# Kernel tuning notes

Hardware: AMD Instinct MI355X
Metric: run time of the kernel (lower is better)

Reference implementation:

```python
import jax, jax.numpy as jnp
import numpy as np

# Grid / physics constants (stand-ins for the attributes of self.model)
N = 256                 # voxels per axis (cubic unit cell)
CELL = 100.0            # unit cell edge in Angstrom (orthogonal cell, frac matrix = I/CELL)
SPACING = CELL / N      # voxel spacing in Angstrom
SOLVENT_R = 1.1         # dilation probe radius (init default `radius`)
EROSION_R = 0.9         # erosion radius (init default `erosion_radius`)
VDW_MAX = 1.9           # static upper bound on vdw radii (generation range [1.2,1.9])
N_ATOMS = 5000


def setup_inputs() -> dict:
    key = jax.random.key(0)
    k1, k2 = jax.random.split(key)
    xyz = jax.random.uniform(k1, (N_ATOMS, 3), jnp.float32) * CELL
    vdw_radii = 1.2 + 0.7 * jax.random.uniform(k2, (N_ATOMS,), jnp.float32)
    return {"xyz": xyz, "vdw_radii": vdw_radii}


def _solvent_pipeline(xyz, vdw_radii):
    # ---- Step 1: dilation -- per-atom radius query into the voxel grid ----
    max_r = VDW_MAX + SOLVENT_R                       # self.max_radius_angstrom
    Kh = int(np.ceil(max_r / SPACING))
    g = np.arange(-Kh, Kh + 1)
    offs = np.stack(np.meshgrid(g, g, g, indexing='ij'), -1).reshape(-1, 3)
    offs = jnp.asarray(offs, jnp.int32)               # [M,3] local voxel offsets

    base = jnp.floor(xyz / SPACING).astype(jnp.int32)          # [A,3] home voxel
    coords = base[:, None, :] + offs[None, :, :]               # [A,M,3]
    centers = coords.astype(jnp.float32) * SPACING             # voxel centers (unwrapped)
    d = jnp.sqrt(jnp.sum((centers - xyz[:, None, :]) ** 2, -1))  # [A,M] atom-voxel dist

    w = jnp.mod(coords, N)                                     # periodic wrap of indices
    flat = ((w[..., 0] * N + w[..., 1]) * N + w[..., 2]).ravel()

    vr = vdw_radii[:, None]
    prot = (d < vr).ravel()                                    # inside vdw -> protein core
    bound = ((d >= vr) & (d < vr + SOLVENT_R)).ravel()         # vdw..vdw+probe -> boundary

    protein = (jnp.zeros(N ** 3, jnp.int8).at[flat].max(prot.astype(jnp.int8)) > 0)
    boundary = (jnp.zeros(N ** 3, jnp.int8).at[flat].max(bound.astype(jnp.int8)) > 0)
    protein = protein.reshape(N, N, N)
    boundary = boundary.reshape(N, N, N) & ~protein            # symmetry = identity (P1)
    def_solv = ~(protein | boundary)

    # ---- Step 2: erosion -- boundary voxel flips to solvent if any voxel within
    #      erosion_radius is definitely solvent ----
    rh = int(np.ceil(EROSION_R / SPACING))
    g2 = np.arange(-rh, rh + 1)
    eo = np.stack(np.meshgrid(g2, g2, g2, indexing='ij'), -1).reshape(-1, 3)
    eo = eo[np.linalg.norm(eo * SPACING, axis=1) <= EROSION_R]  # sphere stencil (static)
    has_nb = jnp.zeros((N, N, N), bool)
    for o in eo:  # small static stencil (~50 offsets)
        has_nb = has_nb | jnp.roll(def_solv, shift=(-int(o[0]), -int(o[1]), -int(o[2])), axis=(0, 1, 2))
    flip = boundary & has_nb
    protein_with_boundary = (protein | boundary) & ~flip
    solvent = (~protein_with_boundary).astype(jnp.float32)

    # ---- Step 3: Gaussian smoothing with circular padding ----
    sigma = (SOLVENT_R / SPACING) / 4.0                        # self.transition (voxels)
    ks = int(4 * sigma + 1)
    if ks % 2 == 0:
        ks += 1
    x = np.arange(ks) - ks // 2
    g1 = np.exp(-x ** 2 / (2 * sigma ** 2))
    g1 = g1 / g1.sum()
    k3 = g1[:, None, None] * g1[None, :, None] * g1[None, None, :]
    k3 = jnp.asarray(k3 / k3.sum(), jnp.float32)
    pad = ks // 2
    padded = jnp.pad(solvent, pad, mode='wrap')
    out = jax.lax.conv_general_dilated(padded[None, None], k3[None, None], (1, 1, 1), 'VALID')
    return out[0, 0]  # [N,N,N] smoothed solvent mask


def reference(xyz, vdw_radii):
    return _solvent_pipeline(xyz, vdw_radii)
```

## Files before the change

kernel.cpp:

```cpp
#include <hip/hip_runtime.h>
#include <math.h>

#define NG 256
#define NG3 (NG*NG*NG)
#define NW (NG3/64)

typedef unsigned long long u64;
typedef unsigned int u32;

constexpr float SPACING_F = 0.390625f;
constexpr int KH = 8;
constexpr int KD = 17;
constexpr int NPAIR = KD * KD;

#define CB(x, y) (((((x) & 255) << 8) | ((y) & 255)) << 2)

__global__ void __launch_bounds__(256) splat_bits_kernel(
    const float* __restrict__ xyz, const float* __restrict__ vdw,
    u64* __restrict__ occ_bits, u64* __restrict__ p_bits, int natoms)
{
    int t = blockIdx.x * 256 + threadIdx.x;
    if (t >= natoms * NPAIR) return;
    int atom = t / NPAIR;
    int pr = t - atom * NPAIR;
    int dx = pr / KD - KH;
    int dy = pr - (pr / KD) * KD - KH;

    const float ax = xyz[atom * 3 + 0];
    const float ay = xyz[atom * 3 + 1];
    const float az = xyz[atom * 3 + 2];
    const float vr = vdw[atom];
    const float br = __fadd_rn(vr, 1.1f);
    const int bx = (int)floorf(__fdiv_rn(ax, SPACING_F));
    const int by = (int)floorf(__fdiv_rn(ay, SPACING_F));
    const int bz = (int)floorf(__fdiv_rn(az, SPACING_F));

    const int cx = bx + dx, cy = by + dy;
    float ex = __fsub_rn(__fmul_rn((float)cx, SPACING_F), ax);
    float ey = __fsub_rn(__fmul_rn((float)cy, SPACING_F), ay);
    float rxy2 = __fadd_rn(__fmul_rn(ex, ex), __fmul_rn(ey, ey));
    if (rxy2 >= __fmul_rn(br, br)) return;

    u32 mo = 0, mp = 0;
    #pragma unroll
    for (int k = 0; k < KD; ++k) {
        int cz = bz + k - KH;
        float ez = __fsub_rn(__fmul_rn((float)cz, SPACING_F), az);
        float s = __fadd_rn(rxy2, __fmul_rn(ez, ez));
        float d = __fsqrt_rn(s);
        mo |= (d < br) ? (1u << k) : 0u;
        mp |= (d < vr) ? (1u << k) : 0u;
    }
    if (!mo) return;

    const int cb = CB(cx, cy);
    const int zA = (bz - KH) & 255;
    const int wa = zA >> 6;
    const int off = zA & 63;

    u64 lo = (u64)mo << off;
    u64 hi = off ? ((u64)mo >> (64 - off)) : 0ULL;
    if (lo) atomicOr(&occ_bits[cb | wa], lo);
    if (hi) atomicOr(&occ_bits[cb | ((wa + 1) & 3)], hi);
    if (mp) {
        u64 plo = (u64)mp << off;
        u64 phi = off ? ((u64)mp >> (64 - off)) : 0ULL;
        if (plo) atomicOr(&p_bits[cb | wa], plo);
        if (phi) atomicOr(&p_bits[cb | ((wa + 1) & 3)], phi);
    }
}

__device__ __forceinline__ u64 rng5(const u64* __restrict__ B, int cb, int wz) {
    u64 C = B[cb | wz], P = B[cb | ((wz + 3) & 3)], Nw = B[cb | ((wz + 1) & 3)];
    u64 d1 = (C << 1) | (P >> 63), d2 = (C << 2) | (P >> 62);
    u64 u1 = (C >> 1) | (Nw << 63), u2 = (C >> 2) | (Nw << 62);
    return C & d1 & d2 & u1 & u2;
}
__device__ __forceinline__ u64 rng3(const u64* __restrict__ B, int cb, int wz) {
    u64 C = B[cb | wz], P = B[cb | ((wz + 3) & 3)], Nw = B[cb | ((wz + 1) & 3)];
    u64 d1 = (C << 1) | (P >> 63);
    u64 u1 = (C >> 1) | (Nw << 63);
    return C & d1 & u1;
}

__global__ void __launch_bounds__(256) solvent_bits_kernel(
    const u64* __restrict__ occ_bits, const u64* __restrict__ p_bits,
    u64* __restrict__ sol_bits)
{
    int w = blockIdx.x * 256 + threadIdx.x;
    int wz = w & 3, col = w >> 2;
    int y = col & 255, x = col >> 8;

    u64 ero = rng5(occ_bits, CB(x, y), wz);
    ero &= rng5(occ_bits, CB(x + 1, y), wz);
    ero &= rng5(occ_bits, CB(x - 1, y), wz);
    ero &= rng5(occ_bits, CB(x, y + 1), wz);
    ero &= rng5(occ_bits, CB(x, y - 1), wz);
    ero &= rng3(occ_bits, CB(x + 1, y + 1), wz);
    ero &= rng3(occ_bits, CB(x + 1, y - 1), wz);
    ero &= rng3(occ_bits, CB(x - 1, y + 1), wz);
    ero &= rng3(occ_bits, CB(x - 1, y - 1), wz);
    ero &= rng3(occ_bits, CB(x + 2, y), wz);
    ero &= rng3(occ_bits, CB(x - 2, y), wz);
    ero &= rng3(occ_bits, CB(x, y + 2), wz);
    ero &= rng3(occ_bits, CB(x, y - 2), wz);
    ero &= occ_bits[CB(x + 1, y + 2) | wz];
    ero &= occ_bits[CB(x + 1, y - 2) | wz];
    ero &= occ_bits[CB(x - 1, y + 2) | wz];
    ero &= occ_bits[CB(x - 1, y - 2) | wz];
    ero &= occ_bits[CB(x + 2, y + 1) | wz];
    ero &= occ_bits[CB(x + 2, y - 1) | wz];
    ero &= occ_bits[CB(x - 2, y + 1) | wz];
    ero &= occ_bits[CB(x - 2, y - 1) | wz];

    u64 occw = occ_bits[w];
    u64 pw = p_bits[w];
    sol_bits[w] = ~(pw | (occw & ero));
}

struct Tri { u64 m1, m0, p1; };
__device__ __forceinline__ Tri tri(const u64* __restrict__ B, int x, int y, int wz) {
    int cb = CB(x, y);
    u64 C = B[cb | wz], P = B[cb | ((wz + 3) & 3)], Nw = B[cb | ((wz + 1) & 3)];
    Tri t;
    t.m0 = C;
    t.m1 = (C << 1) | (P >> 63);
    t.p1 = (C >> 1) | (Nw << 63);
    return t;
}

__global__ void __launch_bounds__(256) gauss_bits_kernel(
    const u64* __restrict__ S, float* __restrict__ out,
    float W0, float W1, float W2, float W3)
{
    __shared__ float lds[256][33];
    const int tid = threadIdx.x;
    const int w = blockIdx.x * 256 + tid;
    const int wz = w & 3, col = w >> 2;
    const int y = col & 255, x = col >> 8;

    Tri cc = tri(S, x, y, wz);
    Tri e0 = tri(S, x + 1, y, wz), e1 = tri(S, x - 1, y, wz);
    Tri e2 = tri(S, x, y + 1, wz), e3 = tri(S, x, y - 1, wz);
    Tri d0 = tri(S, x + 1, y + 1, wz), d1 = tri(S, x + 1, y - 1, wz);
    Tri d2 = tri(S, x - 1, y + 1, wz), d3 = tri(S, x - 1, y - 1, wz);

    float* blk_out = out + (size_t)blockIdx.x * 256 * 64;

    #pragma unroll
    for (int h = 0; h < 2; ++h) {
        const int sh = h * 32;
        u32 g0 = (u32)(cc.m0 >> sh);
        u32 a1[6]  = { (u32)(cc.m1 >> sh), (u32)(cc.p1 >> sh),
                       (u32)(e0.m0 >> sh), (u32)(e1.m0 >> sh),
                       (u32)(e2.m0 >> sh), (u32)(e3.m0 >> sh) };
        u32 a2[12] = { (u32)(e0.m1 >> sh), (u32)(e0.p1 >> sh),
                       (u32)(e1.m1 >> sh), (u32)(e1.p1 >> sh),
                       (u32)(e2.m1 >> sh), (u32)(e2.p1 >> sh),
                       (u32)(e3.m1 >> sh), (u32)(e3.p1 >> sh),
                       (u32)(d0.m0 >> sh), (u32)(d1.m0 >> sh),
                       (u32)(d2.m0 >> sh), (u32)(d3.m0 >> sh) };
        u32 a3[8]  = { (u32)(d0.m1 >> sh), (u32)(d0.p1 >> sh),
                       (u32)(d1.m1 >> sh), (u32)(d1.p1 >> sh),
                       (u32)(d2.m1 >> sh), (u32)(d2.p1 >> sh),
                       (u32)(d3.m1 >> sh), (u32)(d3.p1 >> sh) };
        #pragma unroll
        for (int z = 0; z < 32; ++z) {
            int c1 = 0, c2 = 0, c3 = 0;
            #pragma unroll
            for (int i = 0; i < 6; ++i)  c1 += (a1[i] >> z) & 1;
            #pragma unroll
            for (int i = 0; i < 12; ++i) c2 += (a2[i] >> z) & 1;
            #pragma unroll
            for (int i = 0; i < 8; ++i)  c3 += (a3[i] >> z) & 1;
            float acc = ((g0 >> z) & 1) ? W0 : 0.0f;
            acc = fmaf(W1, (float)c1, acc);
            acc = fmaf(W2, (float)c2, acc);
            acc = fmaf(W3, (float)c3, acc);
            lds[tid][z] = acc;
        }
        __syncthreads();
        #pragma unroll
        for (int k = 0; k < 8; ++k) {
            int i = tid + k * 256;
            int wl = i >> 3;
            int zo = (i & 7) * 4;
            float4 v = make_float4(lds[wl][zo], lds[wl][zo + 1],
                                   lds[wl][zo + 2], lds[wl][zo + 3]);
            *(float4*)(blk_out + (size_t)wl * 64 + sh + zo) = v;
        }
        __syncthreads();
    }
}

extern "C" void kernel_launch(void* const* d_in, const int* in_sizes, int n_in,
                              void* d_out, int out_size, void* d_ws, size_t ws_size,
                              hipStream_t stream)
{
    const float* xyz = (const float*)d_in[0];
    const float* vdw = (const float*)d_in[1];
    float* out = (float*)d_out;

    u64* occ_bits = (u64*)d_ws;
    u64* p_bits   = occ_bits + NW;
    u64* sol_bits = p_bits + NW;
    const int natoms = in_sizes[1];

    hipMemsetAsync(occ_bits, 0, 2 * NW * sizeof(u64), stream);

    int nthreads = natoms * NPAIR;
    splat_bits_kernel<<<(nthreads + 255) / 256, 256, 0, stream>>>(
        xyz, vdw, occ_bits, p_bits, natoms);
    solvent_bits_kernel<<<NW / 256, 256, 0, stream>>>(occ_bits, p_bits, sol_bits);

    double spacing = 100.0 / 256.0;
    double sigma = 1.1 / spacing / 4.0;
    double a = exp(-1.0 / (2.0 * sigma * sigma));
    double ssum = 2.0 * a + 1.0;
    double an = a / ssum, bn = 1.0 / ssum;
    float W0 = (float)(bn * bn * bn);
    float W1 = (float)(an * bn * bn);
    float W2 = (float)(an * an * bn);
    float W3 = (float)(an * an * an);

    gauss_bits_kernel<<<NW / 256, 256, 0, stream>>>(sol_bits, out, W0, W1, W2, W3);
}
```

Baseline: 141.2 us.

## Use bit-sliced carry-save adders and a LUT for Gaussian neighbor counts

Computes the per-voxel counts of face, edge and corner neighbours for the 3x3x3 Gaussian using bitwise carry-save adder trees across 64 z-bits at once, instead of counting each bit per z position. The two bit-sliced counts plus the centre bit then index a 256-entry shared-memory table of partial weighted sums, and the corner count is added with one FMA. This removes most of the per-voxel shift/mask/add work in the gauss kernel, at the cost of an extra LDS table, a block barrier and random-index LDS reads.

After: 119.8 us. 15.2% less time.

```diff
diff --git a/kernel.cpp b/kernel.cpp
--- a/kernel.cpp
+++ b/kernel.cpp
@@ -129,12 +129,28 @@
     return t;
 }
 
+__device__ __forceinline__ void csa(u64 a, u64 b, u64 c, u64& s, u64& cy) {
+    u64 t = a ^ b;
+    s = t ^ c;
+    cy = (a & b) | (t & c);
+}
+
 __global__ void __launch_bounds__(256) gauss_bits_kernel(
     const u64* __restrict__ S, float* __restrict__ out,
     float W0, float W1, float W2, float W3)
 {
+    __shared__ float lutA[256];
     __shared__ float lds[256][33];
     const int tid = threadIdx.x;
+    {
+        int g = tid & 1, c1v = (tid >> 1) & 7, c2v = (tid >> 4) & 15;
+        float acc = g ? W0 : 0.0f;
+        acc = fmaf(W1, (float)c1v, acc);
+        acc = fmaf(W2, (float)c2v, acc);
+        lutA[tid] = acc;
+    }
+    __syncthreads();
+
     const int w = blockIdx.x * 256 + tid;
     const int wz = w & 3, col = w >> 2;
     const int y = col & 255, x = col >> 8;
@@ -145,39 +161,63 @@
     Tri d0 = tri(S, x + 1, y + 1, wz), d1 = tri(S, x + 1, y - 1, wz);
     Tri d2 = tri(S, x - 1, y + 1, wz), d3 = tri(S, x - 1, y - 1, wz);
 
+    u64 sa, ca, sb, cb2;
+    csa(cc.m1, cc.p1, e0.m0, sa, ca);
+    csa(e1.m0, e2.m0, e3.m0, sb, cb2);
+    u64 c1b0 = sa ^ sb; u64 h = sa & sb;
+    u64 c1b1, c1b2;
+    csa(ca, cb2, h, c1b1, c1b2);
+
+    u64 s1, k1, s2, k2, s3, k3, s4, k4;
+    csa(e0.m1, e0.p1, e1.m1, s1, k1);
+    csa(e1.p1, e2.m1, e2.p1, s2, k2);
+    csa(e3.m1, e3.p1, d0.m0, s3, k3);
+    csa(d1.m0, d2.m0, d3.m0, s4, k4);
+    u64 t5, kt;
+    csa(s1, s2, s3, t5, kt);
+    u64 c2b0 = t5 ^ s4; u64 h0 = t5 & s4;
+    u64 u_, ku, v_, kv;
+    csa(k1, k2, k3, u_, ku);
+    csa(k4, kt, h0, v_, kv);
+    u64 c2b1 = u_ ^ v_; u64 h1 = u_ & v_;
+    u64 c2b2, c2b3;
+    csa(ku, kv, h1, c2b2, c2b3);
+
+    u64 p1s, p1c, p2s, p2c;
+    csa(d0.m1, d0.p1, d1.m1, p1s, p1c);
+    csa(d1.p1, d2.m1, d2.p1, p2s, p2c);
+    u64 t3, kt3;
+    csa(p1s, p2s, d3.m1, t3, kt3);
+    u64 c3b0 = t3 ^ d3.p1; u64 h3 = t3 & d3.p1;
+    u64 u3, ku3;
+    csa(p1c, p2c, kt3, u3, ku3);
+    u64 c3b1 = u3 ^ h3; u64 h4 = u3 & h3;
+    u64 c3b2 = ku3 ^ h4, c3b3 = ku3 & h4;
+
     float* blk_out = out + (size_t)blockIdx.x * 256 * 64;
 
     #pragma unroll
-    for (int h = 0; h < 2; ++h) {
-        const int sh = h * 32;
-        u32 g0 = (u32)(cc.m0 >> sh);
-        u32 a1[6]  = { (u32)(cc.m1 >> sh), (u32)(cc.p1 >> sh),
-                       (u32)(e0.m0 >> sh), (u32)(e1.m0 >> sh),
-                       (u32)(e2.m0 >> sh), (u32)(e3.m0 >> sh) };
-        u32 a2[12] = { (u32)(e0.m1 >> sh), (u32)(e0.p1 >> sh),
-                       (u32)(e1.m1 >> sh), (u32)(e1.p1 >> sh),
-                       (u32)(e2.m1 >> sh), (u32)(e2.p1 >> sh),
-                       (u32)(e3.m1 >> sh), (u32)(e3.p1 >> sh),
-                       (u32)(d0.m0 >> sh), (u32)(d1.m0 >> sh),
-                       (u32)(d2.m0 >> sh), (u32)(d3.m0 >> sh) };
-        u32 a3[8]  = { (u32)(d0.m1 >> sh), (u32)(d0.p1 >> sh),
-                       (u32)(d1.m1 >> sh), (u32)(d1.p1 >> sh),
-                       (u32)(d2.m1 >> sh), (u32)(d2.p1 >> sh),
-                       (u32)(d3.m1 >> sh), (u32)(d3.p1 >> sh) };
+    for (int hh = 0; hh < 2; ++hh) {
+        const int sh = hh * 32;
+        u32 pA[8] = { (u32)(cc.m0 >> sh), (u32)(c1b0 >> sh), (u32)(c1b1 >> sh),
+                      (u32)(c1b2 >> sh), (u32)(c2b0 >> sh), (u32)(c2b1 >> sh),
+                      (u32)(c2b2 >> sh), (u32)(c2b3 >> sh) };
+        u32 pB[4] = { (u32)(c3b0 >> sh), (u32)(c3b1 >> sh),
+                      (u32)(c3b2 >> sh), (u32)(c3b3 >> sh) };
         #pragma unroll
-        for (int z = 0; z < 32; ++z) {
-            int c1 = 0, c2 = 0, c3 = 0;
+        for (int z0 = 0; z0 < 8; ++z0) {
+            u32 accA = 0, accB = 0;
             #pragma unroll
-            for (int i = 0; i < 6; ++i)  c1 += (a1[i] >> z) & 1;
+            for (int j = 0; j < 8; ++j) accA |= ((pA[j] >> z0) & 0x01010101u) << j;
             #pragma unroll
-            for (int i = 0; i < 12; ++i) c2 += (a2[i] >> z) & 1;
+            for (int j = 0; j < 4; ++j) accB |= ((pB[j] >> z0) & 0x01010101u) << j;
             #pragma unroll
-            for (int i = 0; i < 8; ++i)  c3 += (a3[i] >> z) & 1;
-            float acc = ((g0 >> z) & 1) ? W0 : 0.0f;
-            acc = fmaf(W1, (float)c1, acc);
-            acc = fmaf(W2, (float)c2, acc);
-            acc = fmaf(W3, (float)c3, acc);
-            lds[tid][z] = acc;
+            for (int b = 0; b < 4; ++b) {
+                int idxA = (accA >> (8 * b)) & 255;
+                int c3v  = (accB >> (8 * b)) & 15;
+                float val = fmaf(W3, (float)c3v, lutA[idxA]);
+                lds[tid][z0 + 8 * b] = val;
+            }
         }
         __syncthreads();
         #pragma unroll
```
